# Kernel optimization log

Measured on AMD Instinct MI355X. Metric: run time of the kernel, lower is better.

Reference implementation:

```python
import jax, jax.numpy as jnp
import numpy as np

B, C, D, H, W = 4, 256, 16, 16, 16


def setup_inputs() -> dict:
    key = jax.random.key(0)
    ks = jax.random.split(key, 9)
    s = 1.0 / np.sqrt(C)
    inp = {
        "x": jax.random.normal(ks[0], (B, C, D, H, W), dtype=jnp.float32),
        "wq": jax.random.normal(ks[1], (C, C), dtype=jnp.float32) * s,
        "bq": jax.random.normal(ks[2], (C,), dtype=jnp.float32) * 0.02,
        "wk": jax.random.normal(ks[3], (C, C), dtype=jnp.float32) * s,
        "bk": jax.random.normal(ks[4], (C,), dtype=jnp.float32) * 0.02,
        "wv": jax.random.normal(ks[5], (C, C), dtype=jnp.float32) * s,
        "bv": jax.random.normal(ks[6], (C,), dtype=jnp.float32) * 0.02,
        "wp": jax.random.normal(ks[7], (C, C), dtype=jnp.float32) * s,
        "bp": jax.random.normal(ks[8], (C,), dtype=jnp.float32) * 0.02,
    }
    return inp


def reference(x, wq, bq, wk, bk, wv, bv, wp, bp):
    b, c, d, h, w = x.shape
    xf = x.reshape(b, c, d * h * w)  # (B, C, N)
    # 1x1 Conv3d == per-voxel linear map over channels
    q = jnp.einsum('oc,bcn->bon', wq, xf) + bq[:, None]
    k = jnp.einsum('oc,bcn->bon', wk, xf) + bk[:, None]
    v = jnp.einsum('oc,bcn->bon', wv, xf) + bv[:, None]
    # scores[b,i,j] = q[:, :, i] . k[:, :, j], scaled AFTER the bmm (as in source)
    scores = jnp.einsum('bci,bcj->bij', q, k) * (c ** -0.5)
    p = jax.nn.softmax(scores, axis=2)  # (B, N, N), softmax over keys j
    # attention[b,c,i] = sum_j v[b,c,j] * p[b,i,j]
    attn = jnp.einsum('bcj,bij->bci', v, p)
    out = jnp.einsum('oc,bcn->bon', wp, attn) + bp[:, None]
    return x + out.reshape(b, c, d, h, w)
```

## Files before the change

kernel.cpp:

```cpp
#include <hip/hip_runtime.h>

typedef unsigned short u16;
typedef unsigned int u32;
typedef __bf16 v8bf __attribute__((ext_vector_type(8)));
typedef float v4f __attribute__((ext_vector_type(4)));

#define DEV __device__ __forceinline__

constexpr int CB = 4;
constexpr int C = 256;
constexpr int NN = 4096;
constexpr float LOG2E = 1.4426950408889634f;

DEV u16 f2bf(float f) {
  union { float f; u32 u; } v; v.f = f;
  u32 r = v.u + 0x7fffu + ((v.u >> 16) & 1u);
  return (u16)(r >> 16);
}
DEV float bf2f(u16 h) {
  union { u32 u; float f; } v; v.u = ((u32)h) << 16; return v.f;
}

DEV void dma16(const u16* g, const u16* lds_base) {
  __builtin_amdgcn_global_load_lds(
      (const __attribute__((address_space(1))) void*)(unsigned long long)g,
      (__attribute__((address_space(3))) void*)(u32)(unsigned long long)lds_base,
      16, 0, 0);
}

__global__ __launch_bounds__(256) void k_transpose(const float* __restrict__ x,
                                                   u16* __restrict__ xT) {
  __shared__ float tile[32][33];
  int b = blockIdx.z;
  int n0 = blockIdx.x * 32, c0 = blockIdx.y * 32;
  int tx = threadIdx.x & 31, ty = threadIdx.x >> 5;
  const float* xb = x + (long)b * C * NN;
#pragma unroll
  for (int r = 0; r < 4; ++r)
    tile[ty + r * 8][tx] = xb[(long)(c0 + ty + r * 8) * NN + n0 + tx];
  __syncthreads();
  u16* xTb = xT + (long)b * NN * C;
#pragma unroll
  for (int r = 0; r < 4; ++r)
    xTb[(long)(n0 + ty + r * 8) * C + c0 + tx] = f2bf(tile[tx][ty + r * 8]);
}

__global__ __launch_bounds__(256) void k_cvt4(const float* __restrict__ s0,
                                              const float* __restrict__ s1,
                                              const float* __restrict__ s2,
                                              const float* __restrict__ s3,
                                              u16* __restrict__ d0, u16* __restrict__ d1,
                                              u16* __restrict__ d2, u16* __restrict__ d3,
                                              float* __restrict__ Mbuf) {
  if (blockIdx.x == 0 && blockIdx.y == 0 && threadIdx.x < 8) Mbuf[threadIdx.x] = 0.f;
  int wsel = blockIdx.y;
  const float* s = wsel == 0 ? s0 : wsel == 1 ? s1 : wsel == 2 ? s2 : s3;
  u16* d = wsel == 0 ? d0 : wsel == 1 ? d1 : wsel == 2 ? d2 : d3;
  int i = blockIdx.x * 256 + threadIdx.x;
  d[i] = f2bf(s[i]);
}

DEV void stage_tile(const u16* __restrict__ g, u16* lds, int t) {
#pragma unroll
  for (int i = 0; i < 8; ++i) {
    int id = t + i * 256;
    int row = id >> 5, ch = id & 31;
    *reinterpret_cast<float4*>(lds + row * 264 + ch * 8) =
        *reinterpret_cast<const float4*>(g + row * 256 + ch * 8);
  }
}

__global__ __launch_bounds__(256) void k_qkv(
    const u16* __restrict__ xT, const u16* __restrict__ wqb, const u16* __restrict__ wkb,
    const u16* __restrict__ wvb, const float* __restrict__ bq, const float* __restrict__ bk,
    const float* __restrict__ bv, u16* __restrict__ qO, u16* __restrict__ kO,
    u16* __restrict__ vO) {
  __shared__ __align__(16) u16 Ash[64 * 264];
  __shared__ __align__(16) u16 Bsh[64 * 264];
  int t = threadIdx.x, w = t >> 6, lane = t & 63, lr = lane & 15, q = lane >> 4;
  int m0 = blockIdx.x * 64, n0 = blockIdx.y * 64, b = blockIdx.z;
  stage_tile(xT + (long)b * NN * C + (long)m0 * 256, Ash, t);
#pragma unroll 1
  for (int wsel = 0; wsel < 3; ++wsel) {
    const u16* wptr = wsel == 0 ? wqb : wsel == 1 ? wkb : wvb;
    stage_tile(wptr + (long)n0 * 256, Bsh, t);
    __syncthreads();
    v4f acc[4];
#pragma unroll
    for (int nt = 0; nt < 4; ++nt)
#pragma unroll
      for (int r = 0; r < 4; ++r) acc[nt][r] = 0.f;
#pragma unroll
    for (int ks = 0; ks < 8; ++ks) {
      v8bf a = *reinterpret_cast<const v8bf*>(Ash + (w * 16 + lr) * 264 + ks * 32 + q * 8);
#pragma unroll
      for (int nt = 0; nt < 4; ++nt) {
        v8bf bb = *reinterpret_cast<const v8bf*>(Bsh + (nt * 16 + lr) * 264 + ks * 32 + q * 8);
        acc[nt] = __builtin_amdgcn_mfma_f32_16x16x32_bf16(a, bb, acc[nt], 0, 0, 0);
      }
    }
    const float* bias = wsel == 0 ? bq : wsel == 1 ? bk : bv;
#pragma unroll
    for (int nt = 0; nt < 4; ++nt) {
#pragma unroll
      for (int r = 0; r < 4; ++r) {
        int gm = m0 + w * 16 + q * 4 + r;
        int gn = n0 + nt * 16 + lr;
        float val = acc[nt][r] + bias[gn];
        if (wsel == 0) {
          qO[((long)b * NN + gm) * C + gn] = f2bf(val * (0.0625f * LOG2E));
        } else if (wsel == 1) {
          kO[((long)b * NN + gm) * C + gn] = f2bf(val);
        } else {
          vO[(long)b * C * NN + (long)gn * NN + gm] = f2bf(val);
        }
      }
    }
    __syncthreads();
  }
}

__global__ __launch_bounds__(256) void k_maxnorm(const u16* __restrict__ qT,
                                                 const u16* __restrict__ kT,
                                                 float* __restrict__ Mbuf) {
  int b = blockIdx.z, tsel = blockIdx.y;
  const u16* src = (tsel ? kT : qT) + (long)b * NN * C;
  int row = blockIdx.x * 64 + (threadIdx.x >> 2);
  const uint4* pp =
      reinterpret_cast<const uint4*>(src + (long)row * C + (threadIdx.x & 3) * 64);
  float s = 0.f;
#pragma unroll
  for (int u = 0; u < 8; ++u) {
    uint4 d = pp[u];
    const u16* e = reinterpret_cast<const u16*>(&d);
#pragma unroll
    for (int i = 0; i < 8; ++i) { float f = bf2f(e[i]); s += f * f; }
  }
  s += __shfl_xor(s, 1, 64);
  s += __shfl_xor(s, 2, 64);
#pragma unroll
  for (int d2 = 4; d2 < 64; d2 <<= 1) s = fmaxf(s, __shfl_xor(s, d2, 64));
  if ((threadIdx.x & 63) == 0)
    atomicMax((u32*)(Mbuf + tsel * 4 + b), __float_as_uint(s));
}

__global__ __launch_bounds__(256) void k_gemm(
    const u16* __restrict__ A, long aStr, const u16* __restrict__ Bm, long bStr,
    const float* __restrict__ biasM, const float* __restrict__ biasN,
    const float* __restrict__ resid, long rStr, float scale,
    float* __restrict__ outF, u16* __restrict__ outH, long oStr, int ldm, int ldn) {
  __shared__ __align__(16) u16 Ash[64 * 264];
  __shared__ __align__(16) u16 Bsh[64 * 264];
  int t = threadIdx.x;
  int w = t >> 6, lane = t & 63, lr = lane & 15, q = lane >> 4;
  int m0 = blockIdx.x * 64, n0 = blockIdx.y * 64, b = blockIdx.z;
  stage_tile(A + b * aStr + (long)m0 * 256, Ash, t);
  stage_tile(Bm + b * bStr + (long)n0 * 256, Bsh, t);
  __syncthreads();
  v4f acc[4];
#pragma unroll
  for (int nt = 0; nt < 4; ++nt)
#pragma unroll
    for (int r = 0; r < 4; ++r) acc[nt][r] = 0.f;
#pragma unroll
  for (int ks = 0; ks < 8; ++ks) {
    v8bf a = *reinterpret_cast<const v8bf*>(Ash + (w * 16 + lr) * 264 + ks * 32 + q * 8);
#pragma unroll
    for (int nt = 0; nt < 4; ++nt) {
      v8bf bb = *reinterpret_cast<const v8bf*>(Bsh + (nt * 16 + lr) * 264 + ks * 32 + q * 8);
      acc[nt] = __builtin_amdgcn_mfma_f32_16x16x32_bf16(a, bb, acc[nt], 0, 0, 0);
    }
  }
#pragma unroll
  for (int nt = 0; nt < 4; ++nt) {
#pragma unroll
    for (int r = 0; r < 4; ++r) {
      int gm = m0 + w * 16 + q * 4 + r;
      int gn = n0 + nt * 16 + lr;
      float val = acc[nt][r];
      if (biasM) val += biasM[gm];
      if (biasN) val += biasN[gn];
      val *= scale;
      long addr = b * oStr + (long)gm * ldm + (long)gn * ldn;
      if (resid) val += resid[b * rStr + (long)gm * ldm + (long)gn * ldn];
      if (outF) outF[addr] = val;
      else outH[addr] = f2bf(val);
    }
  }
}

DEV void flash_issue(const u16* kb, const u16* vb, const u16* kshb, const u16* vshb,
                     int j0, int w, int lane) {
#pragma unroll
  for (int i = 0; i < 4; ++i) {
    int idx = w * 4 + i;
    int kr = idx * 2 + (lane >> 5);
    int kc = (lane & 31) ^ (kr & 7);
    dma16(kb + (long)(j0 + kr) * 256 + kc * 8, kshb + idx * 512);
  }
#pragma unroll
  for (int i = 0; i < 4; ++i) {
    int idx = w * 4 + i;
    int vr = idx * 16 + (lane >> 2);
    int vc = (lane & 3) ^ ((vr ^ (vr >> 2)) & 3);
    dma16(vb + (long)vr * NN + j0 + vc * 8, vshb + idx * 512);
  }
}

__global__ __launch_bounds__(256, 2) void k_flash(const u16* __restrict__ qT,
                                                  const u16* __restrict__ kT,
                                                  const u16* __restrict__ V,
                                                  u16* __restrict__ op0,
                                                  u16* __restrict__ op1,
                                                  u16* __restrict__ op2,
                                                  u16* __restrict__ op3,
                                                  float* __restrict__ ml,
                                                  const float* __restrict__ Mbuf,
                                                  int span) {
  __shared__ __align__(16) u16 ksh[2][32 * 256];
  __shared__ __align__(16) u16 vsh[2][256 * 32];
  __shared__ __align__(16) u16 psh[4 * 16 * 40];
  int t = threadIdx.x;
  int w = t >> 6, lane = t & 63, lr = lane & 15, q = lane >> 4;
  int b = blockIdx.z, h = blockIdx.y;
  int i0 = blockIdx.x * 64;
  const u16* qb = qT + ((long)b * NN + i0 + w * 16) * C;
  const u16* kb = kT + (long)b * NN * C;
  const u16* vb = V + (long)b * C * NN;
  float M = sqrtf(Mbuf[b] * Mbuf[4 + b]) + 1.0f;

  v8bf qf[8];
#pragma unroll
  for (int ks = 0; ks < 8; ++ks)
    qf[ks] = *reinterpret_cast<const v8bf*>(qb + lr * C + ks * 32 + q * 8);

  v4f accO[16];
#pragma unroll
  for (int ct = 0; ct < 16; ++ct)
#pragma unroll
    for (int r = 0; r < 4; ++r) accO[ct][r] = 0.f;
  float lsum[4] = {0.f, 0.f, 0.f, 0.f};

  u16* pw = psh + w * 640;
  const int xk = lr & 7;
  const int xv = (lr ^ (lr >> 2)) & 3;

  int jstart = h * span;
  int niter = span >> 5;
  flash_issue(kb, vb, ksh[0], vsh[0], jstart, w, lane);
  int cur = 0;
#pragma unroll 1
  for (int it = 0; it < niter; ++it) {
    int j0 = jstart + (it << 5);
    int jn = (it + 1 < niter) ? j0 + 32 : jstart;
    asm volatile("s_waitcnt lgkmcnt(0)\n\ts_barrier" ::: "memory");
    flash_issue(kb, vb, ksh[cur ^ 1], vsh[cur ^ 1], jn, w, lane);
    asm volatile("s_waitcnt vmcnt(8)\n\ts_barrier" ::: "memory");

    const u16* kcur = ksh[cur];
    const u16* vcur = vsh[cur];
    v4f s[2];
#pragma unroll
    for (int jt = 0; jt < 2; ++jt)
#pragma unroll
      for (int r = 0; r < 4; ++r) s[jt][r] = 0.f;
#pragma unroll
    for (int ks = 0; ks < 8; ++ks) {
#pragma unroll
      for (int jt = 0; jt < 2; ++jt) {
        v8bf kf = *reinterpret_cast<const v8bf*>(
            kcur + (jt * 16 + lr) * 256 + (((ks * 4 + q) ^ xk) << 3));
        s[jt] = __builtin_amdgcn_mfma_f32_16x16x32_bf16(qf[ks], kf, s[jt], 0, 0, 0);
      }
    }

#pragma unroll
    for (int jt = 0; jt < 2; ++jt) {
#pragma unroll
      for (int r = 0; r < 4; ++r) {
        float p = exp2f(s[jt][r] - M);
        lsum[r] += p;
        u32 pb = (__float_as_uint(p) + 0x8000u) >> 16;
        pw[(q * 4 + r) * 40 + jt * 16 + lr] = (u16)pb;
      }
    }
    asm volatile("s_waitcnt lgkmcnt(0)" ::: "memory");
    v8bf pa = *reinterpret_cast<const v8bf*>(pw + lr * 40 + q * 8);
#pragma unroll
    for (int ct = 0; ct < 16; ++ct) {
      v8bf v0 = *reinterpret_cast<const v8bf*>(
          vcur + (ct * 16 + lr) * 32 + ((q ^ xv) << 3));
      accO[ct] = __builtin_amdgcn_mfma_f32_16x16x32_bf16(pa, v0, accO[ct], 0, 0, 0);
    }
    cur ^= 1;
  }

#pragma unroll
  for (int r = 0; r < 4; ++r) {
#pragma unroll
    for (int d = 1; d < 16; d <<= 1) lsum[r] += __shfl_xor(lsum[r], d, 64);
  }
  float inv[4];
#pragma unroll
  for (int r = 0; r < 4; ++r) inv[r] = 1.0f / lsum[r];
  u16* opp = h == 0 ? op0 : h == 1 ? op1 : h == 2 ? op2 : op3;
  u16* ob = opp + ((long)b * NN + i0 + w * 16) * C;
#pragma unroll
  for (int ct = 0; ct < 16; ++ct)
#pragma unroll
    for (int r = 0; r < 4; ++r)
      ob[(q * 4 + r) * C + ct * 16 + lr] = f2bf(accO[ct][r] * inv[r]);
  if (lr == 0) {
    long rbase = ((long)h * CB + b) * NN + i0 + w * 16 + q * 4;
#pragma unroll
    for (int r = 0; r < 4; ++r) {
      ml[(rbase + r) * 2] = M;
      ml[(rbase + r) * 2 + 1] = lsum[r];
    }
  }
}

__global__ __launch_bounds__(256) void k_combine(const u16* __restrict__ p0,
                                                 const u16* __restrict__ p1,
                                                 const u16* __restrict__ p2,
                                                 const u16* __restrict__ p3,
                                                 const float* __restrict__ ml,
                                                 u16* __restrict__ o, int js) {
  long row = (long)blockIdx.x * 8 + (threadIdx.x >> 5);
  int tc = (threadIdx.x & 31) * 8;
  float m[4], l[4];
  float mx = -3.0e38f;
  for (int h = 0; h < js; ++h) {
    m[h] = ml[((long)h * CB * NN + row) * 2];
    l[h] = ml[((long)h * CB * NN + row) * 2 + 1];
    mx = fmaxf(mx, m[h]);
  }
  float tot = 0.f, a[4];
  for (int h = 0; h < js; ++h) { a[h] = exp2f(m[h] - mx) * l[h]; tot += a[h]; }
  float inv = 1.f / tot;
  float acc[8];
#pragma unroll
  for (int i = 0; i < 8; ++i) acc[i] = 0.f;
  const u16* ps[4] = {p0, p1, p2, p3};
  for (int h = 0; h < js; ++h) {
    uint4 u = *reinterpret_cast<const uint4*>(ps[h] + row * C + tc);
    const u16* p = reinterpret_cast<const u16*>(&u);
    float wgt = a[h] * inv;
#pragma unroll
    for (int i = 0; i < 8; ++i) acc[i] += wgt * bf2f(p[i]);
  }
  u16 outv[8];
#pragma unroll
  for (int i = 0; i < 8; ++i) outv[i] = f2bf(acc[i]);
  *reinterpret_cast<uint4*>(o + row * C + tc) = *reinterpret_cast<const uint4*>(outv);
}

extern "C" void kernel_launch(void* const* d_in, const int* in_sizes, int n_in,
                              void* d_out, int out_size, void* d_ws, size_t ws_size,
                              hipStream_t stream) {
  const float* x = (const float*)d_in[0];
  const float* wq = (const float*)d_in[1];
  const float* bq = (const float*)d_in[2];
  const float* wk = (const float*)d_in[3];
  const float* bk = (const float*)d_in[4];
  const float* wv = (const float*)d_in[5];
  const float* bv = (const float*)d_in[6];
  const float* wp = (const float*)d_in[7];
  const float* bp = (const float*)d_in[8];
  float* out = (float*)d_out;
  char* ws = (char*)d_ws;

  const long SLOT = 8388608L;
  const size_t NEED4 = 524288UL + 7 * 8388608UL + 524288UL + 4096UL;
  int js = (ws_size >= NEED4) ? 4 : 2;

  u16* wqb = (u16*)(ws + 0);
  u16* wkb = (u16*)(ws + 131072L);
  u16* wvb = (u16*)(ws + 262144L);
  u16* wpb = (u16*)(ws + 393216L);
  char* base = ws + 524288L;
  u16* xT  = (u16*)(base);
  u16* qTw = (u16*)(base + 1 * SLOT);
  u16* kTw = (u16*)(base + 2 * SLOT);
  u16* vw  = (u16*)(base + 3 * SLOT);
  u16* op1 = (u16*)(base + 4 * SLOT);
  u16* op2 = js == 4 ? (u16*)(base + 5 * SLOT) : op1;
  u16* op3 = js == 4 ? (u16*)(base + 6 * SLOT) : op1;
  float* ml = (float*)(base + (js == 4 ? 7 : 5) * SLOT);
  float* Mbuf = ml + 131072;
  u16* op0 = xT;
  u16* oW  = qTw;

  k_cvt4<<<dim3(256, 4), 256, 0, stream>>>(wq, wk, wv, wp, wqb, wkb, wvb, wpb, Mbuf);
  k_transpose<<<dim3(128, 8, CB), 256, 0, stream>>>(x, xT);
  k_qkv<<<dim3(64, 4, CB), 256, 0, stream>>>(xT, wqb, wkb, wvb, bq, bk, bv, qTw, kTw, vw);
  k_maxnorm<<<dim3(64, 2, CB), 256, 0, stream>>>(qTw, kTw, Mbuf);
  k_flash<<<dim3(64, js, CB), 256, 0, stream>>>(qTw, kTw, vw, op0, op1, op2, op3, ml,
                                                Mbuf, NN / js);
  k_combine<<<2048, 256, 0, stream>>>(op0, op1, op2, op3, ml, oW, js);

  long nc = (long)NN * C;
  k_gemm<<<dim3(4, 64, CB), 256, 0, stream>>>(wpb, 0, oW, nc, bp, nullptr, x, nc,
                                              1.0f, out, nullptr, nc, NN, 1);
}
```

Measured before the change: 274.0 us.

## Fuse preprocessing into QKV, use 32x32 MFMA flash, fuse combine into projection

The separate transpose, weight-convert and max-norm kernels are folded into the QKV kernel. It now reads fp32 x and the weights directly, converts them to bf16 in LDS, and computes the per-tile squared-norm bound in its epilogue. The flash kernel moves from 16x16x32 to 32x32x16 MFMAs with 128 query rows per block and a single global softmax offset, so split partials combine using only the row sums. The combine step and the output projection plus residual are merged into one kernel, which removes the intermediate bf16 buffer and several launches. The looser global norm bound (sum of per-tile maxima) could lower exp precision, and the larger per-wave register footprint may affect occupancy.

```diff
diff --git a/kernel.cpp b/kernel.cpp
--- a/kernel.cpp
+++ b/kernel.cpp
@@ -4,6 +4,7 @@
 typedef unsigned int u32;
 typedef __bf16 v8bf __attribute__((ext_vector_type(8)));
 typedef float v4f __attribute__((ext_vector_type(4)));
+typedef float v16f __attribute__((ext_vector_type(16)));
 
 #define DEV __device__ __forceinline__
 
@@ -28,62 +29,47 @@
       16, 0, 0);
 }
 
-__global__ __launch_bounds__(256) void k_transpose(const float* __restrict__ x,
-                                                   u16* __restrict__ xT) {
-  __shared__ float tile[32][33];
-  int b = blockIdx.z;
-  int n0 = blockIdx.x * 32, c0 = blockIdx.y * 32;
-  int tx = threadIdx.x & 31, ty = threadIdx.x >> 5;
-  const float* xb = x + (long)b * C * NN;
-#pragma unroll
-  for (int r = 0; r < 4; ++r)
-    tile[ty + r * 8][tx] = xb[(long)(c0 + ty + r * 8) * NN + n0 + tx];
-  __syncthreads();
-  u16* xTb = xT + (long)b * NN * C;
-#pragma unroll
-  for (int r = 0; r < 4; ++r)
-    xTb[(long)(n0 + ty + r * 8) * C + c0 + tx] = f2bf(tile[tx][ty + r * 8]);
-}
-
-__global__ __launch_bounds__(256) void k_cvt4(const float* __restrict__ s0,
-                                              const float* __restrict__ s1,
-                                              const float* __restrict__ s2,
-                                              const float* __restrict__ s3,
-                                              u16* __restrict__ d0, u16* __restrict__ d1,
-                                              u16* __restrict__ d2, u16* __restrict__ d3,
-                                              float* __restrict__ Mbuf) {
-  if (blockIdx.x == 0 && blockIdx.y == 0 && threadIdx.x < 8) Mbuf[threadIdx.x] = 0.f;
-  int wsel = blockIdx.y;
-  const float* s = wsel == 0 ? s0 : wsel == 1 ? s1 : wsel == 2 ? s2 : s3;
-  u16* d = wsel == 0 ? d0 : wsel == 1 ? d1 : wsel == 2 ? d2 : d3;
-  int i = blockIdx.x * 256 + threadIdx.x;
-  d[i] = f2bf(s[i]);
-}
-
-DEV void stage_tile(const u16* __restrict__ g, u16* lds, int t) {
-#pragma unroll
-  for (int i = 0; i < 8; ++i) {
-    int id = t + i * 256;
-    int row = id >> 5, ch = id & 31;
-    *reinterpret_cast<float4*>(lds + row * 264 + ch * 8) =
-        *reinterpret_cast<const float4*>(g + row * 256 + ch * 8);
-  }
-}
-
 __global__ __launch_bounds__(256) void k_qkv(
-    const u16* __restrict__ xT, const u16* __restrict__ wqb, const u16* __restrict__ wkb,
-    const u16* __restrict__ wvb, const float* __restrict__ bq, const float* __restrict__ bk,
+    const float* __restrict__ x, const float* __restrict__ wq,
+    const float* __restrict__ wk, const float* __restrict__ wv,
+    const float* __restrict__ bq, const float* __restrict__ bk,
     const float* __restrict__ bv, u16* __restrict__ qO, u16* __restrict__ kO,
-    u16* __restrict__ vO) {
+    u16* __restrict__ vO, float* __restrict__ Mbuf) {
   __shared__ __align__(16) u16 Ash[64 * 264];
   __shared__ __align__(16) u16 Bsh[64 * 264];
   int t = threadIdx.x, w = t >> 6, lane = t & 63, lr = lane & 15, q = lane >> 4;
-  int m0 = blockIdx.x * 64, n0 = blockIdx.y * 64, b = blockIdx.z;
-  stage_tile(xT + (long)b * NN * C + (long)m0 * 256, Ash, t);
+  int n0 = blockIdx.x * 64, ot = blockIdx.y, b = blockIdx.z;
+  const float* xb = x + (long)b * C * NN;
+
+  {
+    int col = t & 63, grp = t >> 6;
+#pragma unroll
+    for (int rep = 0; rep < 8; ++rep) {
+      int cbase = grp * 8 + rep * 32;
+      u16 pk[8];
+#pragma unroll
+      for (int j = 0; j < 8; ++j)
+        pk[j] = f2bf(xb[(long)(cbase + j) * NN + n0 + col]);
+      *reinterpret_cast<uint4*>(Ash + col * 264 + cbase) =
+          *reinterpret_cast<const uint4*>(pk);
+    }
+  }
+  __syncthreads();
+
 #pragma unroll 1
   for (int wsel = 0; wsel < 3; ++wsel) {
-    const u16* wptr = wsel == 0 ? wqb : wsel == 1 ? wkb : wvb;
-    stage_tile(wptr + (long)n0 * 256, Bsh, t);
+    const float* W = wsel == 0 ? wq : wsel == 1 ? wk : wv;
+    const float* bias = wsel == 0 ? bq : wsel == 1 ? bk : bv;
+#pragma unroll
+    for (int i = 0; i < 8; ++i) {
+      int id = t + i * 256, row = id >> 5, ch = id & 31;
+      const float4* wp4 = reinterpret_cast<const float4*>(W + (long)(ot * 64 + row) * C + ch * 8);
+      float4 f0 = wp4[0], f1 = wp4[1];
+      u16 pk[8] = {f2bf(f0.x), f2bf(f0.y), f2bf(f0.z), f2bf(f0.w),
+                   f2bf(f1.x), f2bf(f1.y), f2bf(f1.z), f2bf(f1.w)};
+      *reinterpret_cast<uint4*>(Bsh + row * 264 + ch * 8) =
+          *reinterpret_cast<const uint4*>(pk);
+    }
     __syncthreads();
     v4f acc[4];
 #pragma unroll
@@ -99,260 +85,248 @@
         acc[nt] = __builtin_amdgcn_mfma_f32_16x16x32_bf16(a, bb, acc[nt], 0, 0, 0);
       }
     }
-    const float* bias = wsel == 0 ? bq : wsel == 1 ? bk : bv;
+    float rp[4] = {0.f, 0.f, 0.f, 0.f};
 #pragma unroll
     for (int nt = 0; nt < 4; ++nt) {
 #pragma unroll
       for (int r = 0; r < 4; ++r) {
-        int gm = m0 + w * 16 + q * 4 + r;
-        int gn = n0 + nt * 16 + lr;
+        int gm = n0 + w * 16 + q * 4 + r;
+        int gn = ot * 64 + nt * 16 + lr;
         float val = acc[nt][r] + bias[gn];
         if (wsel == 0) {
-          qO[((long)b * NN + gm) * C + gn] = f2bf(val * (0.0625f * LOG2E));
+          val *= (0.0625f * LOG2E);
+          qO[((long)b * NN + gm) * C + gn] = f2bf(val);
+          rp[r] += val * val;
         } else if (wsel == 1) {
           kO[((long)b * NN + gm) * C + gn] = f2bf(val);
+          rp[r] += val * val;
         } else {
           vO[(long)b * C * NN + (long)gn * NN + gm] = f2bf(val);
         }
       }
     }
+    if (wsel < 2) {
+      float mx = 0.f;
+#pragma unroll
+      for (int r = 0; r < 4; ++r) {
+#pragma unroll
+        for (int d = 1; d < 16; d <<= 1) rp[r] += __shfl_xor(rp[r], d, 64);
+        mx = fmaxf(mx, rp[r]);
+      }
+      mx = fmaxf(mx, __shfl_xor(mx, 16, 64));
+      mx = fmaxf(mx, __shfl_xor(mx, 32, 64));
+      if (lane == 0) atomicMax((u32*)(Mbuf + wsel * 4 + ot), __float_as_uint(mx));
+    }
     __syncthreads();
-  }
-}
-
-__global__ __launch_bounds__(256) void k_maxnorm(const u16* __restrict__ qT,
-                                                 const u16* __restrict__ kT,
-                                                 float* __restrict__ Mbuf) {
-  int b = blockIdx.z, tsel = blockIdx.y;
-  const u16* src = (tsel ? kT : qT) + (long)b * NN * C;
-  int row = blockIdx.x * 64 + (threadIdx.x >> 2);
-  const uint4* pp =
-      reinterpret_cast<const uint4*>(src + (long)row * C + (threadIdx.x & 3) * 64);
-  float s = 0.f;
-#pragma unroll
-  for (int u = 0; u < 8; ++u) {
-    uint4 d = pp[u];
-    const u16* e = reinterpret_cast<const u16*>(&d);
-#pragma unroll
-    for (int i = 0; i < 8; ++i) { float f = bf2f(e[i]); s += f * f; }
-  }
-  s += __shfl_xor(s, 1, 64);
-  s += __shfl_xor(s, 2, 64);
-#pragma unroll
-  for (int d2 = 4; d2 < 64; d2 <<= 1) s = fmaxf(s, __shfl_xor(s, d2, 64));
-  if ((threadIdx.x & 63) == 0)
-    atomicMax((u32*)(Mbuf + tsel * 4 + b), __float_as_uint(s));
-}
-
-__global__ __launch_bounds__(256) void k_gemm(
-    const u16* __restrict__ A, long aStr, const u16* __restrict__ Bm, long bStr,
-    const float* __restrict__ biasM, const float* __restrict__ biasN,
-    const float* __restrict__ resid, long rStr, float scale,
-    float* __restrict__ outF, u16* __restrict__ outH, long oStr, int ldm, int ldn) {
-  __shared__ __align__(16) u16 Ash[64 * 264];
-  __shared__ __align__(16) u16 Bsh[64 * 264];
-  int t = threadIdx.x;
-  int w = t >> 6, lane = t & 63, lr = lane & 15, q = lane >> 4;
-  int m0 = blockIdx.x * 64, n0 = blockIdx.y * 64, b = blockIdx.z;
-  stage_tile(A + b * aStr + (long)m0 * 256, Ash, t);
-  stage_tile(Bm + b * bStr + (long)n0 * 256, Bsh, t);
-  __syncthreads();
-  v4f acc[4];
-#pragma unroll
-  for (int nt = 0; nt < 4; ++nt)
-#pragma unroll
-    for (int r = 0; r < 4; ++r) acc[nt][r] = 0.f;
-#pragma unroll
-  for (int ks = 0; ks < 8; ++ks) {
-    v8bf a = *reinterpret_cast<const v8bf*>(Ash + (w * 16 + lr) * 264 + ks * 32 + q * 8);
-#pragma unroll
-    for (int nt = 0; nt < 4; ++nt) {
-      v8bf bb = *reinterpret_cast<const v8bf*>(Bsh + (nt * 16 + lr) * 264 + ks * 32 + q * 8);
-      acc[nt] = __builtin_amdgcn_mfma_f32_16x16x32_bf16(a, bb, acc[nt], 0, 0, 0);
-    }
-  }
-#pragma unroll
-  for (int nt = 0; nt < 4; ++nt) {
-#pragma unroll
-    for (int r = 0; r < 4; ++r) {
-      int gm = m0 + w * 16 + q * 4 + r;
-      int gn = n0 + nt * 16 + lr;
-      float val = acc[nt][r];
-      if (biasM) val += biasM[gm];
-      if (biasN) val += biasN[gn];
-      val *= scale;
-      long addr = b * oStr + (long)gm * ldm + (long)gn * ldn;
-      if (resid) val += resid[b * rStr + (long)gm * ldm + (long)gn * ldn];
-      if (outF) outF[addr] = val;
-      else outH[addr] = f2bf(val);
-    }
   }
 }
 
 DEV void flash_issue(const u16* kb, const u16* vb, const u16* kshb, const u16* vshb,
                      int j0, int w, int lane) {
+  int h5 = lane >> 5, l31 = lane & 31;
 #pragma unroll
   for (int i = 0; i < 4; ++i) {
     int idx = w * 4 + i;
-    int kr = idx * 2 + (lane >> 5);
-    int kc = (lane & 31) ^ (kr & 7);
-    dma16(kb + (long)(j0 + kr) * 256 + kc * 8, kshb + idx * 512);
+    int j = idx * 2 + h5;
+    int kc = (l31 ^ (j & 7)) * 8;
+    dma16(kb + (long)(j0 + j) * C + kc, kshb + idx * 512);
   }
 #pragma unroll
   for (int i = 0; i < 4; ++i) {
     int idx = w * 4 + i;
-    int vr = idx * 16 + (lane >> 2);
-    int vc = (lane & 3) ^ ((vr ^ (vr >> 2)) & 3);
-    dma16(vb + (long)vr * NN + j0 + vc * 8, vshb + idx * 512);
-  }
-}
-
-__global__ __launch_bounds__(256, 2) void k_flash(const u16* __restrict__ qT,
-                                                  const u16* __restrict__ kT,
-                                                  const u16* __restrict__ V,
-                                                  u16* __restrict__ op0,
-                                                  u16* __restrict__ op1,
-                                                  u16* __restrict__ op2,
-                                                  u16* __restrict__ op3,
-                                                  float* __restrict__ ml,
-                                                  const float* __restrict__ Mbuf,
-                                                  int span) {
+    int c = idx * 16 + (lane >> 2);
+    int vc = ((lane & 3) ^ (c & 3)) * 8;
+    dma16(vb + (long)c * NN + j0 + vc, vshb + idx * 512);
+  }
+}
+
+__global__ __launch_bounds__(256, 2) void k_flash(
+    const u16* __restrict__ qT, const u16* __restrict__ kT, const u16* __restrict__ V,
+    u16* __restrict__ op0, u16* __restrict__ op1, u16* __restrict__ op2,
+    u16* __restrict__ op3, float* __restrict__ lsum, const float* __restrict__ Mbuf,
+    int span) {
   __shared__ __align__(16) u16 ksh[2][32 * 256];
   __shared__ __align__(16) u16 vsh[2][256 * 32];
-  __shared__ __align__(16) u16 psh[4 * 16 * 40];
+  __shared__ __align__(16) u16 psh[4 * 32 * 40];
   int t = threadIdx.x;
-  int w = t >> 6, lane = t & 63, lr = lane & 15, q = lane >> 4;
+  int w = t >> 6, lane = t & 63, h5 = lane >> 5, l31 = lane & 31;
   int b = blockIdx.z, h = blockIdx.y;
-  int i0 = blockIdx.x * 64;
-  const u16* qb = qT + ((long)b * NN + i0 + w * 16) * C;
+  int i0 = blockIdx.x * 128;
   const u16* kb = kT + (long)b * NN * C;
   const u16* vb = V + (long)b * C * NN;
-  float M = sqrtf(Mbuf[b] * Mbuf[4 + b]) + 1.0f;
-
-  v8bf qf[8];
-#pragma unroll
-  for (int ks = 0; ks < 8; ++ks)
-    qf[ks] = *reinterpret_cast<const v8bf*>(qb + lr * C + ks * 32 + q * 8);
-
-  v4f accO[16];
-#pragma unroll
-  for (int ct = 0; ct < 16; ++ct)
-#pragma unroll
-    for (int r = 0; r < 4; ++r) accO[ct][r] = 0.f;
-  float lsum[4] = {0.f, 0.f, 0.f, 0.f};
-
-  u16* pw = psh + w * 640;
-  const int xk = lr & 7;
-  const int xv = (lr ^ (lr >> 2)) & 3;
-
+  float Sq = Mbuf[0] + Mbuf[1] + Mbuf[2] + Mbuf[3];
+  float Sk = Mbuf[4] + Mbuf[5] + Mbuf[6] + Mbuf[7];
+  float M = sqrtf(Sq * Sk) + 0.5f;
+
+  const u16* qrow = qT + ((long)b * NN + i0 + w * 32 + l31) * C + h5 * 8;
+  v8bf qf[16];
+#pragma unroll
+  for (int ck = 0; ck < 16; ++ck)
+    qf[ck] = *reinterpret_cast<const v8bf*>(qrow + ck * 16);
+
+  v16f accO[8];
+#pragma unroll
+  for (int ct = 0; ct < 8; ++ct)
+#pragma unroll
+    for (int r = 0; r < 16; ++r) accO[ct][r] = 0.f;
+  float lsm[16];
+#pragma unroll
+  for (int r = 0; r < 16; ++r) lsm[r] = 0.f;
+
+  u16* pw = psh + w * 1280;
   int jstart = h * span;
   int niter = span >> 5;
   flash_issue(kb, vb, ksh[0], vsh[0], jstart, w, lane);
   int cur = 0;
 #pragma unroll 1
   for (int it = 0; it < niter; ++it) {
-    int j0 = jstart + (it << 5);
-    int jn = (it + 1 < niter) ? j0 + 32 : jstart;
+    int jn = (it + 1 < niter) ? jstart + ((it + 1) << 5) : jstart;
     asm volatile("s_waitcnt lgkmcnt(0)\n\ts_barrier" ::: "memory");
     flash_issue(kb, vb, ksh[cur ^ 1], vsh[cur ^ 1], jn, w, lane);
     asm volatile("s_waitcnt vmcnt(8)\n\ts_barrier" ::: "memory");
 
     const u16* kcur = ksh[cur];
     const u16* vcur = vsh[cur];
-    v4f s[2];
-#pragma unroll
-    for (int jt = 0; jt < 2; ++jt)
-#pragma unroll
-      for (int r = 0; r < 4; ++r) s[jt][r] = 0.f;
+    v16f s;
+#pragma unroll
+    for (int r = 0; r < 16; ++r) s[r] = 0.f;
+#pragma unroll
+    for (int ck = 0; ck < 16; ++ck) {
+      int pos = ((ck * 2 + h5) ^ (l31 & 7)) * 8;
+      v8bf kf = *reinterpret_cast<const v8bf*>(kcur + l31 * 256 + pos);
+      s = __builtin_amdgcn_mfma_f32_32x32x16_bf16(qf[ck], kf, s, 0, 0, 0);
+    }
+
+#pragma unroll
+    for (int r = 0; r < 16; ++r) {
+      float p = exp2f(s[r] - M);
+      lsm[r] += p;
+      u32 pb = (__float_as_uint(p) + 0x8000u) >> 16;
+      int irow = (r & 3) + 8 * (r >> 2) + 4 * h5;
+      pw[irow * 40 + l31] = (u16)pb;
+    }
+    asm volatile("s_waitcnt lgkmcnt(0)" ::: "memory");
+
+#pragma unroll
+    for (int kh = 0; kh < 2; ++kh) {
+      v8bf pa = *reinterpret_cast<const v8bf*>(pw + l31 * 40 + kh * 16 + h5 * 8);
+#pragma unroll
+      for (int ct = 0; ct < 8; ++ct) {
+        int c = ct * 32 + l31;
+        int pos = ((kh * 2 + h5) ^ (c & 3)) * 8;
+        v8bf vf = *reinterpret_cast<const v8bf*>(vcur + c * 32 + pos);
+        accO[ct] = __builtin_amdgcn_mfma_f32_32x32x16_bf16(pa, vf, accO[ct], 0, 0, 0);
+      }
+    }
+    cur ^= 1;
+  }
+
+#pragma unroll
+  for (int r = 0; r < 16; ++r) {
+#pragma unroll
+    for (int d = 1; d < 32; d <<= 1) lsm[r] += __shfl_xor(lsm[r], d, 64);
+  }
+  float invl[16];
+#pragma unroll
+  for (int r = 0; r < 16; ++r) invl[r] = 1.0f / lsm[r];
+
+  u16* opp = h == 0 ? op0 : h == 1 ? op1 : h == 2 ? op2 : op3;
+  u16* ob = opp + ((long)b * NN + i0 + w * 32) * C;
+#pragma unroll
+  for (int ct = 0; ct < 8; ++ct)
+#pragma unroll
+    for (int r = 0; r < 16; ++r) {
+      int irow = (r & 3) + 8 * (r >> 2) + 4 * h5;
+      ob[(long)irow * C + ct * 32 + l31] = f2bf(accO[ct][r] * invl[r]);
+    }
+  if (l31 == 0) {
+    float* lb2 = lsum + ((long)h * CB + b) * NN + i0 + w * 32;
+#pragma unroll
+    for (int r = 0; r < 16; ++r) {
+      int irow = (r & 3) + 8 * (r >> 2) + 4 * h5;
+      lb2[irow] = lsm[r];
+    }
+  }
+}
+
+__global__ __launch_bounds__(256) void k_out(
+    const u16* __restrict__ p0, const u16* __restrict__ p1, const u16* __restrict__ p2,
+    const u16* __restrict__ p3, const float* __restrict__ lsum,
+    const float* __restrict__ wp, const float* __restrict__ bp,
+    const float* __restrict__ x, float* __restrict__ out, int js) {
+  __shared__ __align__(16) u16 Ash[64 * 264];
+  __shared__ __align__(16) u16 Bsh[64 * 264];
+  int t = threadIdx.x, w = t >> 6, lane = t & 63, lr = lane & 15, q = lane >> 4;
+  int n0 = blockIdx.x * 64, b = blockIdx.y;
+  const u16* ps[4] = {p0, p1, p2, p3};
+
+#pragma unroll
+  for (int i = 0; i < 8; ++i) {
+    int id = t + i * 256, row = id >> 5, ch = id & 31;
+    long nrow = (long)b * NN + n0 + row;
+    float wsum = 0.f, wgt[4];
+    for (int hh = 0; hh < js; ++hh) {
+      wgt[hh] = lsum[(long)hh * CB * NN + nrow];
+      wsum += wgt[hh];
+    }
+    float inv = 1.0f / wsum;
+    float accv[8];
+#pragma unroll
+    for (int j = 0; j < 8; ++j) accv[j] = 0.f;
+    for (int hh = 0; hh < js; ++hh) {
+      uint4 u = *reinterpret_cast<const uint4*>(ps[hh] + nrow * C + ch * 8);
+      const u16* pe = reinterpret_cast<const u16*>(&u);
+      float g = wgt[hh] * inv;
+#pragma unroll
+      for (int j = 0; j < 8; ++j) accv[j] += g * bf2f(pe[j]);
+    }
+    u16 pk[8];
+#pragma unroll
+    for (int j = 0; j < 8; ++j) pk[j] = f2bf(accv[j]);
+    *reinterpret_cast<uint4*>(Bsh + row * 264 + ch * 8) =
+        *reinterpret_cast<const uint4*>(pk);
+  }
+  __syncthreads();
+
+#pragma unroll 1
+  for (int ot = 0; ot < 4; ++ot) {
+#pragma unroll
+    for (int i = 0; i < 8; ++i) {
+      int id = t + i * 256, row = id >> 5, ch = id & 31;
+      const float4* wp4 = reinterpret_cast<const float4*>(wp + (long)(ot * 64 + row) * C + ch * 8);
+      float4 f0 = wp4[0], f1 = wp4[1];
+      u16 pk[8] = {f2bf(f0.x), f2bf(f0.y), f2bf(f0.z), f2bf(f0.w),
+                   f2bf(f1.x), f2bf(f1.y), f2bf(f1.z), f2bf(f1.w)};
+      *reinterpret_cast<uint4*>(Ash + row * 264 + ch * 8) =
+          *reinterpret_cast<const uint4*>(pk);
+    }
+    __syncthreads();
+    v4f acc[4];
+#pragma unroll
+    for (int nt = 0; nt < 4; ++nt)
+#pragma unroll
+      for (int r = 0; r < 4; ++r) acc[nt][r] = 0.f;
 #pragma unroll
     for (int ks = 0; ks < 8; ++ks) {
-#pragma unroll
-      for (int jt = 0; jt < 2; ++jt) {
-        v8bf kf = *reinterpret_cast<const v8bf*>(
-            kcur + (jt * 16 + lr) * 256 + (((ks * 4 + q) ^ xk) << 3));
-        s[jt] = __builtin_amdgcn_mfma_f32_16x16x32_bf16(qf[ks], kf, s[jt], 0, 0, 0);
-      }
-    }
-
-#pragma unroll
-    for (int jt = 0; jt < 2; ++jt) {
+      v8bf a = *reinterpret_cast<const v8bf*>(Ash + (w * 16 + lr) * 264 + ks * 32 + q * 8);
+#pragma unroll
+      for (int nt = 0; nt < 4; ++nt) {
+        v8bf bb = *reinterpret_cast<const v8bf*>(Bsh + (nt * 16 + lr) * 264 + ks * 32 + q * 8);
+        acc[nt] = __builtin_amdgcn_mfma_f32_16x16x32_bf16(a, bb, acc[nt], 0, 0, 0);
+      }
+    }
+#pragma unroll
+    for (int nt = 0; nt < 4; ++nt) {
 #pragma unroll
       for (int r = 0; r < 4; ++r) {
-        float p = exp2f(s[jt][r] - M);
-        lsum[r] += p;
-        u32 pb = (__float_as_uint(p) + 0x8000u) >> 16;
-        pw[(q * 4 + r) * 40 + jt * 16 + lr] = (u16)pb;
-      }
-    }
-    asm volatile("s_waitcnt lgkmcnt(0)" ::: "memory");
-    v8bf pa = *reinterpret_cast<const v8bf*>(pw + lr * 40 + q * 8);
-#pragma unroll
-    for (int ct = 0; ct < 16; ++ct) {
-      v8bf v0 = *reinterpret_cast<const v8bf*>(
-          vcur + (ct * 16 + lr) * 32 + ((q ^ xv) << 3));
-      accO[ct] = __builtin_amdgcn_mfma_f32_16x16x32_bf16(pa, v0, accO[ct], 0, 0, 0);
-    }
-    cur ^= 1;
-  }
-
-#pragma unroll
-  for (int r = 0; r < 4; ++r) {
-#pragma unroll
-    for (int d = 1; d < 16; d <<= 1) lsum[r] += __shfl_xor(lsum[r], d, 64);
-  }
-  float inv[4];
-#pragma unroll
-  for (int r = 0; r < 4; ++r) inv[r] = 1.0f / lsum[r];
-  u16* opp = h == 0 ? op0 : h == 1 ? op1 : h == 2 ? op2 : op3;
-  u16* ob = opp + ((long)b * NN + i0 + w * 16) * C;
-#pragma unroll
-  for (int ct = 0; ct < 16; ++ct)
-#pragma unroll
-    for (int r = 0; r < 4; ++r)
-      ob[(q * 4 + r) * C + ct * 16 + lr] = f2bf(accO[ct][r] * inv[r]);
-  if (lr == 0) {
-    long rbase = ((long)h * CB + b) * NN + i0 + w * 16 + q * 4;
-#pragma unroll
-    for (int r = 0; r < 4; ++r) {
-      ml[(rbase + r) * 2] = M;
-      ml[(rbase + r) * 2 + 1] = lsum[r];
-    }
-  }
-}
-
-__global__ __launch_bounds__(256) void k_combine(const u16* __restrict__ p0,
-                                                 const u16* __restrict__ p1,
-                                                 const u16* __restrict__ p2,
-                                                 const u16* __restrict__ p3,
-                                                 const float* __restrict__ ml,
-                                                 u16* __restrict__ o, int js) {
-  long row = (long)blockIdx.x * 8 + (threadIdx.x >> 5);
-  int tc = (threadIdx.x & 31) * 8;
-  float m[4], l[4];
-  float mx = -3.0e38f;
-  for (int h = 0; h < js; ++h) {
-    m[h] = ml[((long)h * CB * NN + row) * 2];
-    l[h] = ml[((long)h * CB * NN + row) * 2 + 1];
-    mx = fmaxf(mx, m[h]);
-  }
-  float tot = 0.f, a[4];
-  for (int h = 0; h < js; ++h) { a[h] = exp2f(m[h] - mx) * l[h]; tot += a[h]; }
-  float inv = 1.f / tot;
-  float acc[8];
-#pragma unroll
-  for (int i = 0; i < 8; ++i) acc[i] = 0.f;
-  const u16* ps[4] = {p0, p1, p2, p3};
-  for (int h = 0; h < js; ++h) {
-    uint4 u = *reinterpret_cast<const uint4*>(ps[h] + row * C + tc);
-    const u16* p = reinterpret_cast<const u16*>(&u);
-    float wgt = a[h] * inv;
-#pragma unroll
-    for (int i = 0; i < 8; ++i) acc[i] += wgt * bf2f(p[i]);
-  }
-  u16 outv[8];
-#pragma unroll
-  for (int i = 0; i < 8; ++i) outv[i] = f2bf(acc[i]);
-  *reinterpret_cast<uint4*>(o + row * C + tc) = *reinterpret_cast<const uint4*>(outv);
+        int gm = ot * 64 + w * 16 + q * 4 + r;
+        int gn = n0 + nt * 16 + lr;
+        long addr = ((long)b * C + gm) * NN + gn;
+        out[addr] = acc[nt][r] + bp[gm] + x[addr];
+      }
+    }
+    __syncthreads();
+  }
 }
 
 extern "C" void kernel_launch(void* const* d_in, const int* in_sizes, int n_in,
@@ -371,35 +345,22 @@
   char* ws = (char*)d_ws;
 
   const long SLOT = 8388608L;
-  const size_t NEED4 = 524288UL + 7 * 8388608UL + 524288UL + 4096UL;
+  const size_t NEED4 = 7 * 8388608UL + 262144UL + 64UL;
   int js = (ws_size >= NEED4) ? 4 : 2;
 
-  u16* wqb = (u16*)(ws + 0);
-  u16* wkb = (u16*)(ws + 131072L);
-  u16* wvb = (u16*)(ws + 262144L);
-  u16* wpb = (u16*)(ws + 393216L);
-  char* base = ws + 524288L;
-  u16* xT  = (u16*)(base);
-  u16* qTw = (u16*)(base + 1 * SLOT);
-  u16* kTw = (u16*)(base + 2 * SLOT);
-  u16* vw  = (u16*)(base + 3 * SLOT);
-  u16* op1 = (u16*)(base + 4 * SLOT);
-  u16* op2 = js == 4 ? (u16*)(base + 5 * SLOT) : op1;
-  u16* op3 = js == 4 ? (u16*)(base + 6 * SLOT) : op1;
-  float* ml = (float*)(base + (js == 4 ? 7 : 5) * SLOT);
-  float* Mbuf = ml + 131072;
-  u16* op0 = xT;
-  u16* oW  = qTw;
-
-  k_cvt4<<<dim3(256, 4), 256, 0, stream>>>(wq, wk, wv, wp, wqb, wkb, wvb, wpb, Mbuf);
-  k_transpose<<<dim3(128, 8, CB), 256, 0, stream>>>(x, xT);
-  k_qkv<<<dim3(64, 4, CB), 256, 0, stream>>>(xT, wqb, wkb, wvb, bq, bk, bv, qTw, kTw, vw);
-  k_maxnorm<<<dim3(64, 2, CB), 256, 0, stream>>>(qTw, kTw, Mbuf);
-  k_flash<<<dim3(64, js, CB), 256, 0, stream>>>(qTw, kTw, vw, op0, op1, op2, op3, ml,
-                                                Mbuf, NN / js);
-  k_combine<<<2048, 256, 0, stream>>>(op0, op1, op2, op3, ml, oW, js);
-
-  long nc = (long)NN * C;
-  k_gemm<<<dim3(4, 64, CB), 256, 0, stream>>>(wpb, 0, oW, nc, bp, nullptr, x, nc,
-                                              1.0f, out, nullptr, nc, NN, 1);
-}
+  u16* qTw = (u16*)(ws + 0 * SLOT);
+  u16* kTw = (u16*)(ws + 1 * SLOT);
+  u16* vw  = (u16*)(ws + 2 * SLOT);
+  u16* op0 = (u16*)(ws + 3 * SLOT);
+  u16* op1 = (u16*)(ws + 4 * SLOT);
+  u16* op2 = js == 4 ? (u16*)(ws + 5 * SLOT) : op1;
+  u16* op3 = js == 4 ? (u16*)(ws + 6 * SLOT) : op1;
+  float* lsum = (float*)(ws + (js == 4 ? 7 : 5) * SLOT);
+  float* Mbuf = lsum + 4 * CB * NN;
+
+  hipMemsetAsync(Mbuf, 0, 32, stream);
+  k_qkv<<<dim3(64, 4, CB), 256, 0, stream>>>(x, wq, wk, wv, bq, bk, bv, qTw, kTw, vw, Mbuf);
+  k_flash<<<dim3(32, js, CB), 256, 0, stream>>>(qTw, kTw, vw, op0, op1, op2, op3,
+                                                lsum, Mbuf, NN / js);
+  k_out<<<dim3(64, CB), 256, 0, stream>>>(op0, op1, op2, op3, lsum, wp, bp, x, out, js);
+}
```

New measurement: 359.0 us. +31.0%, slower.
